# Performance work log

Measured on AMD Instinct MI355X. Metric: run time of the kernel, lower is better.

## Reference

```python
import jax, jax.numpy as jnp
import numpy as np

B, T = 4096, 2048

def setup_inputs() -> dict:
    key = jax.random.key(0)
    k1, k2, k3 = jax.random.split(key, 3)
    pred = jax.random.normal(k1, (B, T), dtype=jnp.float32)  # predicted log-durations
    # alignment = ground-truth durations (strictly positive, log is taken)
    alignment = jax.random.uniform(k2, (B, T), dtype=jnp.float32, minval=1.0, maxval=20.0)
    token_lengths = jax.random.randint(k3, (B,), 1, T + 1)  # valid lengths in [1, T]
    return {"pred": pred, "alignment": alignment, "token_lengths": token_lengths}

def reference(pred, alignment, token_lengths):
    # Masked per-sample MSE over the first token_lengths[i] positions,
    # then mean over the batch (matches the python loop exactly).
    Tdim = pred.shape[1]
    mask = jnp.arange(Tdim)[None, :] < token_lengths[:, None]          # [B, T] bool
    diff = jnp.where(mask, pred - jnp.log(alignment), 0.0)             # padded alignment > 0, log is safe
    per_sample_mse = jnp.sum(diff * diff, axis=1) / token_lengths.astype(pred.dtype)  # [B]
    return jnp.mean(per_sample_mse)
```

## Files before the change

kernel.cpp:

```cpp
#include <hip/hip_runtime.h>


__global__ __launch_bounds__(1024) void dploss_fused_kernel(
    const float* __restrict__ pred,
    const float* __restrict__ align,
    const int* __restrict__ lens,
    float* __restrict__ out,
    int B, int T)
{
    const int gtid = blockIdx.x * blockDim.x + threadIdx.x;
    const int wave = gtid >> 6;
    const int lane = threadIdx.x & 63;
    const int wave_in_block = threadIdx.x >> 6;

    float row_mse = 0.0f;

    if (wave < B) {
        const int row = wave;
        const int L = lens[row];
        const float* __restrict__ prow = pred  + (size_t)row * T;
        const float* __restrict__ arow = align + (size_t)row * T;
        const float4* __restrict__ p4 = (const float4*)prow;
        const float4* __restrict__ a4 = (const float4*)arow;
        const int nfull = L >> 2;

        float acc = 0.0f;
        #pragma unroll 2
        for (int g = lane; g < nfull; g += 64) {
            float4 p = p4[g];
            float4 a = a4[g];
            float d0 = p.x - __logf(a.x);
            float d1 = p.y - __logf(a.y);
            float d2 = p.z - __logf(a.z);
            float d3 = p.w - __logf(a.w);
            acc += d0 * d0 + d1 * d1 + d2 * d2 + d3 * d3;
        }

        const int rem = L & 3;
        if (lane < rem) {
            const int idx = (nfull << 2) + lane;
            float d = prow[idx] - __logf(arow[idx]);
            acc += d * d;
        }

        #pragma unroll
        for (int off = 32; off > 0; off >>= 1)
            acc += __shfl_down(acc, off, 64);

        row_mse = acc / (float)L;
    }

    __shared__ float wsum[16];
    if (lane == 0) wsum[wave_in_block] = row_mse;
    __syncthreads();

    if (threadIdx.x == 0) {
        float total = 0.0f;
        #pragma unroll
        for (int w = 0; w < 16; ++w) total += wsum[w];
        atomicAdd(out, total / (float)B);
    }
}

extern "C" void kernel_launch(void* const* d_in, const int* in_sizes, int n_in,
                              void* d_out, int out_size, void* d_ws, size_t ws_size,
                              hipStream_t stream)
{
    const float* pred  = (const float*)d_in[0];
    const float* align = (const float*)d_in[1];
    const int*   lens  = (const int*)d_in[2];

    const int B = in_sizes[2];
    const int T = in_sizes[0] / B;

    float* out = (float*)d_out;

    hipMemsetAsync(out, 0, sizeof(float), stream);

    const int threads = 1024;
    const int waves_per_block = threads / 64;
    const int grid = (B + waves_per_block - 1) / waves_per_block;

    dploss_fused_kernel<<<grid, threads, 0, stream>>>(pred, align, lens, out, B, T);
}
```

Before: 95.52 us.

## Assign one 256-thread block per row and reduce row MSEs in second kernel

Each batch row is now handled by a 256-thread block instead of a single wave, so every row gets more parallel loads and the work per row is spread more evenly. Per-row MSE values go to workspace, and a separate single-block kernel sums them, replacing the memset and the global atomic. The cost is an extra kernel launch, a serial final-reduction stage and a workspace round trip.

```diff
diff --git a/kernel.cpp b/kernel.cpp
--- a/kernel.cpp
+++ b/kernel.cpp
@@ -1,64 +1,90 @@
 #include <hip/hip_runtime.h>
 
 
-__global__ __launch_bounds__(1024) void dploss_fused_kernel(
+__global__ __launch_bounds__(256) void dploss_row_kernel(
     const float* __restrict__ pred,
     const float* __restrict__ align,
     const int* __restrict__ lens,
-    float* __restrict__ out,
+    float* __restrict__ row_mse,
     int B, int T)
 {
-    const int gtid = blockIdx.x * blockDim.x + threadIdx.x;
-    const int wave = gtid >> 6;
-    const int lane = threadIdx.x & 63;
-    const int wave_in_block = threadIdx.x >> 6;
+    const int row  = blockIdx.x;
+    const int tid  = threadIdx.x;
+    const int lane = tid & 63;
+    const int wib  = tid >> 6;
 
-    float row_mse = 0.0f;
+    const int L = lens[row];
+    const float* __restrict__ prow = pred  + (size_t)row * T;
+    const float* __restrict__ arow = align + (size_t)row * T;
+    const float4* __restrict__ p4 = (const float4*)prow;
+    const float4* __restrict__ a4 = (const float4*)arow;
+    const int nfull = L >> 2;
 
-    if (wave < B) {
-        const int row = wave;
-        const int L = lens[row];
-        const float* __restrict__ prow = pred  + (size_t)row * T;
-        const float* __restrict__ arow = align + (size_t)row * T;
-        const float4* __restrict__ p4 = (const float4*)prow;
-        const float4* __restrict__ a4 = (const float4*)arow;
-        const int nfull = L >> 2;
-
-        float acc = 0.0f;
-        #pragma unroll 2
-        for (int g = lane; g < nfull; g += 64) {
-            float4 p = p4[g];
-            float4 a = a4[g];
-            float d0 = p.x - __logf(a.x);
-            float d1 = p.y - __logf(a.y);
-            float d2 = p.z - __logf(a.z);
-            float d3 = p.w - __logf(a.w);
-            acc += d0 * d0 + d1 * d1 + d2 * d2 + d3 * d3;
-        }
-
-        const int rem = L & 3;
-        if (lane < rem) {
-            const int idx = (nfull << 2) + lane;
-            float d = prow[idx] - __logf(arow[idx]);
-            acc += d * d;
-        }
-
-        #pragma unroll
-        for (int off = 32; off > 0; off >>= 1)
-            acc += __shfl_down(acc, off, 64);
-
-        row_mse = acc / (float)L;
+    float acc = 0.0f;
+    #pragma unroll 2
+    for (int g = tid; g < nfull; g += 256) {
+        float4 p = p4[g];
+        float4 a = a4[g];
+        float d0 = p.x - __logf(a.x);
+        float d1 = p.y - __logf(a.y);
+        float d2 = p.z - __logf(a.z);
+        float d3 = p.w - __logf(a.w);
+        acc += d0 * d0 + d1 * d1 + d2 * d2 + d3 * d3;
     }
 
-    __shared__ float wsum[16];
-    if (lane == 0) wsum[wave_in_block] = row_mse;
+    const int rem = L & 3;
+    if (tid < rem) {
+        const int idx = (nfull << 2) + tid;
+        float d = prow[idx] - __logf(arow[idx]);
+        acc += d * d;
+    }
+
+    #pragma unroll
+    for (int off = 32; off > 0; off >>= 1)
+        acc += __shfl_down(acc, off, 64);
+
+    __shared__ float wsum[4];
+    if (lane == 0) wsum[wib] = acc;
     __syncthreads();
 
-    if (threadIdx.x == 0) {
+    if (tid == 0) {
+        float s = wsum[0] + wsum[1] + wsum[2] + wsum[3];
+        row_mse[row] = s / (float)L;
+    }
+}
+
+__global__ __launch_bounds__(1024) void dploss_reduce_kernel(
+    const float* __restrict__ row_mse,
+    float* __restrict__ out,
+    int B)
+{
+    const int tid  = threadIdx.x;
+    const int lane = tid & 63;
+    const int wib  = tid >> 6;
+
+    float acc = 0.0f;
+    const int B4 = B >> 2;
+    const float4* __restrict__ r4 = (const float4*)row_mse;
+    for (int g = tid; g < B4; g += 1024) {
+        float4 v = r4[g];
+        acc += v.x + v.y + v.z + v.w;
+    }
+    for (int i = (B4 << 2) + tid; i < B; i += 1024)
+        acc += row_mse[i];
+
+    #pragma unroll
+    for (int off = 32; off > 0; off >>= 1)
+        acc += __shfl_down(acc, off, 64);
+
+    __shared__ float wsum[16];
+    if (lane == 0) wsum[wib] = acc;
+    __syncthreads();
+
+    if (tid == 0) {
         float total = 0.0f;
         #pragma unroll
         for (int w = 0; w < 16; ++w) total += wsum[w];
-        atomicAdd(out, total / (float)B);
+        out[0] = total / (float)B;
     }
 }
 
@@ -73,13 +99,9 @@
     const int B = in_sizes[2];
     const int T = in_sizes[0] / B;
 
-    float* out = (float*)d_out;
+    float* out     = (float*)d_out;
+    float* row_mse = (float*)d_ws;
 
-    hipMemsetAsync(out, 0, sizeof(float), stream);
-
-    const int threads = 1024;
-    const int waves_per_block = threads / 64;
-    const int grid = (B + waves_per_block - 1) / waves_per_block;
-
-    dploss_fused_kernel<<<grid, threads, 0, stream>>>(pred, align, lens, out, B, T);
+    dploss_row_kernel<<<B, 256, 0, stream>>>(pred, align, lens, row_mse, B, T);
+    dploss_reduce_kernel<<<1, 1024, 0, stream>>>(row_mse, out, B);
 }
```

Result: faster. 93.25 us (-2.4%).
